# Optimization experiments

Measured on AMD Instinct MI355X. Metric: run time of the kernel, lower is better.

## Reference

```python
import jax, jax.numpy as jnp
import numpy as np


def setup_inputs() -> dict:
    key = jax.random.key(0)
    k1, = jax.random.split(key, 1)
    inputs = jax.random.normal(k1, (16, 64, 64, 512), dtype=jnp.float32)
    gamma = jnp.zeros((1,), dtype=jnp.float32)
    return {"inputs": inputs, "gamma": gamma}


def reference(inputs, gamma):
    # inputs: [B, H, W, C] (NHWC)
    B, H, W, C = inputs.shape
    vec_a = inputs.reshape(B, H * W, C)              # [B, N, C], N = H*W
    # channel Gram matrix: aTa[b, i, j] = sum_n a[b, n, i] * a[b, n, j]
    aTa = jnp.einsum('bni,bnj->bij', vec_a, vec_a)    # [B, C, C]
    attn = jax.nn.softmax(aTa, axis=-1)               # softmax over last axis
    # aaTa = attn @ vec_a^T -> [B, C, N]; transpose -> [B, N, C]
    aaTa = jnp.einsum('bij,bnj->bni', attn, vec_a)    # [B, N, C]
    aaTa = aaTa.reshape(B, H, W, C)
    return gamma * aaTa + inputs
```

## Files before the change

kernel.cpp:

```cpp
#include <hip/hip_runtime.h>

#define BATCH 16
#define NPIX  4096
#define CCH   512
#define NSPLIT 4
#define KSPL  (NPIX / NSPLIT)

using bf16x8   = __attribute__((ext_vector_type(8))) __bf16;
using floatx4  = __attribute__((ext_vector_type(4))) float;
using ushort8v = __attribute__((ext_vector_type(8))) unsigned short;

static __device__ __forceinline__ unsigned short f2bf(float f) {
    unsigned u = __builtin_bit_cast(unsigned, f);
    unsigned r = 0x7fffu + ((u >> 16) & 1u);
    return (unsigned short)((u + r) >> 16);
}

static __device__ __forceinline__ bf16x8 ld_frag(const unsigned short* p) {
    return __builtin_bit_cast(bf16x8, *(const ushort8v*)p);
}

static __device__ __forceinline__ void gld16(const unsigned short* g, unsigned short* l) {
    __builtin_amdgcn_global_load_lds(
        (const __attribute__((address_space(1))) void*)g,
        (__attribute__((address_space(3))) void*)l,
        16, 0, 0);
}

__global__ __launch_bounds__(256) void k_cvt(const float* __restrict__ inp,
                                             unsigned short* __restrict__ Abf,
                                             unsigned short* __restrict__ AT) {
    __shared__ unsigned short sN[64 * 68];
    const int bn = blockIdx.x;
    const int bc = blockIdx.y;
    const int b  = blockIdx.z;
    const int t  = threadIdx.x;
    const int n0 = bn * 64, c0 = bc * 64;
    const float* ip = inp + ((size_t)b * NPIX + n0) * CCH + c0;
    unsigned short* op = Abf + ((size_t)b * NPIX + n0) * CCH + c0;

#pragma unroll
    for (int r = 0; r < 4; ++r) {
        int n  = r * 16 + (t >> 4);
        int c4 = (t & 15) * 4;
        float4 v = *(const float4*)(ip + (size_t)n * CCH + c4);
        uint2 w;
        w.x = (unsigned)f2bf(v.x) | ((unsigned)f2bf(v.y) << 16);
        w.y = (unsigned)f2bf(v.z) | ((unsigned)f2bf(v.w) << 16);
        *(uint2*)(op + (size_t)n * CCH + c4) = w;
        *(uint2*)&sN[n * 68 + c4] = w;
    }
    __syncthreads();

    const int cp = t >> 3;
    const int ng = (t & 7) * 8;
    ushort8v o0, o1;
#pragma unroll
    for (int k = 0; k < 8; ++k) {
        unsigned d = *(const unsigned*)&sN[(ng + k) * 68 + cp * 2];
        o0[k] = (unsigned short)(d & 0xffffu);
        o1[k] = (unsigned short)(d >> 16);
    }
    unsigned short* tp = AT + ((size_t)b * CCH + c0) * NPIX + n0;
    *(ushort8v*)(tp + (size_t)(cp * 2)     * NPIX + ng) = o0;
    *(ushort8v*)(tp + (size_t)(cp * 2 + 1) * NPIX + ng) = o1;
}

__global__ __launch_bounds__(256) void k_ata(const unsigned short* __restrict__ AT,
                                             float* __restrict__ Sp) {
    __shared__ unsigned short sA[128 * 32];
    __shared__ unsigned short sB[128 * 32];
    const int bi = blockIdx.x, bj = blockIdx.y;
    const int b = blockIdx.z & (BATCH - 1), s = blockIdx.z >> 4;
    const unsigned short* pa = AT + ((size_t)b * CCH + bi * 128) * NPIX + s * KSPL;
    const unsigned short* pb = AT + ((size_t)b * CCH + bj * 128) * NPIX + s * KSPL;
    const int tid = threadIdx.x, lane = tid & 63, wave = tid >> 6;
    const int lrow = lane >> 2;
    const int lk   = (lane & 3) * 8;

    floatx4 acc[2][8];
#pragma unroll
    for (int tm = 0; tm < 2; ++tm)
#pragma unroll
        for (int tn = 0; tn < 8; ++tn)
            acc[tm][tn] = floatx4{0.f, 0.f, 0.f, 0.f};

    for (int k0 = 0; k0 < KSPL; k0 += 32) {
#pragma unroll
        for (int i = 0; i < 2; ++i) {
            const int r = wave * 32 + i * 16;
            gld16(pa + (size_t)(r + lrow) * NPIX + k0 + lk, &sA[r * 32]);
            gld16(pb + (size_t)(r + lrow) * NPIX + k0 + lk, &sB[r * 32]);
        }
        __syncthreads();

        const int kq = (lane >> 4) * 8;
        bf16x8 af[2], bv[8];
#pragma unroll
        for (int tm = 0; tm < 2; ++tm)
            af[tm] = ld_frag(&sA[(wave * 32 + tm * 16 + (lane & 15)) * 32 + kq]);
#pragma unroll
        for (int tn = 0; tn < 8; ++tn)
            bv[tn] = ld_frag(&sB[(tn * 16 + (lane & 15)) * 32 + kq]);
#pragma unroll
        for (int tm = 0; tm < 2; ++tm)
#pragma unroll
            for (int tn = 0; tn < 8; ++tn)
                acc[tm][tn] = __builtin_amdgcn_mfma_f32_16x16x32_bf16(
                    af[tm], bv[tn], acc[tm][tn], 0, 0, 0);
        __syncthreads();
    }

    float* Sb = Sp + (((size_t)s * BATCH + b) * CCH + bi * 128) * CCH + bj * 128;
#pragma unroll
    for (int tm = 0; tm < 2; ++tm)
#pragma unroll
        for (int tn = 0; tn < 8; ++tn)
#pragma unroll
            for (int r = 0; r < 4; ++r) {
                int irow = wave * 32 + tm * 16 + (lane >> 4) * 4 + r;
                int jcol = tn * 16 + (lane & 15);
                Sb[(size_t)irow * CCH + jcol] = acc[tm][tn][r];
            }
}

__global__ __launch_bounds__(256) void k_softmax(const float* __restrict__ Sp,
                                                 unsigned short* __restrict__ P) {
    __shared__ float red[6];
    const size_t row = blockIdx.x;
    const size_t str = (size_t)BATCH * CCH * CCH;
    const float* p = Sp + row * CCH;
    const int tid = threadIdx.x, lane = tid & 63, wave = tid >> 6;

    float x0 = p[tid] + p[str + tid] + p[2 * str + tid] + p[3 * str + tid];
    float x1 = p[tid + 256] + p[str + tid + 256] + p[2 * str + tid + 256] + p[3 * str + tid + 256];
    float m = fmaxf(x0, x1);
#pragma unroll
    for (int o = 32; o; o >>= 1) m = fmaxf(m, __shfl_xor(m, o, 64));
    if (lane == 0) red[wave] = m;
    __syncthreads();
    if (tid == 0) red[4] = fmaxf(fmaxf(red[0], red[1]), fmaxf(red[2], red[3]));
    __syncthreads();
    m = red[4];

    float e0 = __expf(x0 - m), e1 = __expf(x1 - m);
    float sum = e0 + e1;
#pragma unroll
    for (int o = 32; o; o >>= 1) sum += __shfl_xor(sum, o, 64);
    if (lane == 0) red[wave] = sum;
    __syncthreads();
    if (tid == 0) red[5] = red[0] + red[1] + red[2] + red[3];
    __syncthreads();
    float inv = 1.0f / red[5];

    P[row * CCH + tid]       = f2bf(e0 * inv);
    P[row * CCH + tid + 256] = f2bf(e1 * inv);
}

__global__ __launch_bounds__(256) void k_av(const unsigned short* __restrict__ Abf,
                                            const unsigned short* __restrict__ P,
                                            const float* __restrict__ inp,
                                            const float* __restrict__ gamma,
                                            float* __restrict__ out) {
    __shared__ unsigned short sA[128 * 32];
    __shared__ unsigned short sB[128 * 32];
    const int bn = blockIdx.x, bi = blockIdx.y, b = blockIdx.z;
    const unsigned short* pa = Abf + ((size_t)b * NPIX + bn * 128) * CCH;
    const unsigned short* pb = P + ((size_t)b * CCH + bi * 128) * CCH;
    const int tid = threadIdx.x, lane = tid & 63, wave = tid >> 6;
    const int lrow = lane >> 2;
    const int lk   = (lane & 3) * 8;
    const float g = gamma[0];

    floatx4 acc[2][8];
#pragma unroll
    for (int tm = 0; tm < 2; ++tm)
#pragma unroll
        for (int tn = 0; tn < 8; ++tn)
            acc[tm][tn] = floatx4{0.f, 0.f, 0.f, 0.f};

    for (int k0 = 0; k0 < CCH; k0 += 32) {
#pragma unroll
        for (int i = 0; i < 2; ++i) {
            const int r = wave * 32 + i * 16;
            gld16(pa + (size_t)(r + lrow) * CCH + k0 + lk, &sA[r * 32]);
            gld16(pb + (size_t)(r + lrow) * CCH + k0 + lk, &sB[r * 32]);
        }
        __syncthreads();

        const int kq = (lane >> 4) * 8;
        bf16x8 af[2], bv[8];
#pragma unroll
        for (int tm = 0; tm < 2; ++tm)
            af[tm] = ld_frag(&sA[(wave * 32 + tm * 16 + (lane & 15)) * 32 + kq]);
#pragma unroll
        for (int tn = 0; tn < 8; ++tn)
            bv[tn] = ld_frag(&sB[(tn * 16 + (lane & 15)) * 32 + kq]);
#pragma unroll
        for (int tm = 0; tm < 2; ++tm)
#pragma unroll
            for (int tn = 0; tn < 8; ++tn)
                acc[tm][tn] = __builtin_amdgcn_mfma_f32_16x16x32_bf16(
                    af[tm], bv[tn], acc[tm][tn], 0, 0, 0);
        __syncthreads();
    }

    float* Ob = out + ((size_t)b * NPIX + bn * 128) * CCH + bi * 128;
    const float* Ib = inp + ((size_t)b * NPIX + bn * 128) * CCH + bi * 128;
#pragma unroll
    for (int tm = 0; tm < 2; ++tm)
#pragma unroll
        for (int tn = 0; tn < 8; ++tn)
#pragma unroll
            for (int r = 0; r < 4; ++r) {
                int nrow = wave * 32 + tm * 16 + (lane >> 4) * 4 + r;
                int icol = tn * 16 + (lane & 15);
                size_t o = (size_t)nrow * CCH + icol;
                Ob[o] = g * acc[tm][tn][r] + Ib[o];
            }
}

extern "C" void kernel_launch(void* const* d_in, const int* in_sizes, int n_in,
                              void* d_out, int out_size, void* d_ws, size_t ws_size,
                              hipStream_t stream) {
    const float* inp   = (const float*)d_in[0];
    const float* gamma = (const float*)d_in[1];
    float* out = (float*)d_out;

    char* ws = (char*)d_ws;
    unsigned short* Abf = (unsigned short*)ws;
    unsigned short* AT  = (unsigned short*)(ws + (size_t)67108864);
    float*          Sp  = (float*)(ws + (size_t)134217728);
    unsigned short* P   = (unsigned short*)(ws + (size_t)201326592);

    k_cvt<<<dim3(NPIX / 64, CCH / 64, BATCH), 256, 0, stream>>>(inp, Abf, AT);
    k_ata<<<dim3(4, 4, BATCH * NSPLIT), 256, 0, stream>>>(AT, Sp);
    k_softmax<<<BATCH * CCH, 256, 0, stream>>>(Sp, P);
    k_av<<<dim3(NPIX / 128, CCH / 128, BATCH), 256, 0, stream>>>(Abf, P, inp, gamma, out);
}
```

Baseline: 459.0 us.

## Exploit Gram symmetry, store bf16 partials in fragment layout, widen split-K

```diff
diff --git a/kernel.cpp b/kernel.cpp
--- a/kernel.cpp
+++ b/kernel.cpp
@@ -3,23 +3,27 @@
 #define BATCH 16
 #define NPIX  4096
 #define CCH   512
-#define NSPLIT 4
+#define NSPLIT 8
 #define KSPL  (NPIX / NSPLIT)
+#define NUT   10
 
 using bf16x8   = __attribute__((ext_vector_type(8))) __bf16;
 using floatx4  = __attribute__((ext_vector_type(4))) float;
 using ushort8v = __attribute__((ext_vector_type(8))) unsigned short;
+using ushort4v = __attribute__((ext_vector_type(4))) unsigned short;
 
 static __device__ __forceinline__ unsigned short f2bf(float f) {
     unsigned u = __builtin_bit_cast(unsigned, f);
     unsigned r = 0x7fffu + ((u >> 16) & 1u);
     return (unsigned short)((u + r) >> 16);
 }
-
+static __device__ __forceinline__ float bf2f(unsigned short v) {
+    unsigned u = ((unsigned)v) << 16;
+    return __builtin_bit_cast(float, u);
+}
 static __device__ __forceinline__ bf16x8 ld_frag(const unsigned short* p) {
     return __builtin_bit_cast(bf16x8, *(const ushort8v*)p);
 }
-
 static __device__ __forceinline__ void gld16(const unsigned short* g, unsigned short* l) {
     __builtin_amdgcn_global_load_lds(
         (const __attribute__((address_space(1))) void*)g,
@@ -30,25 +34,24 @@
 __global__ __launch_bounds__(256) void k_cvt(const float* __restrict__ inp,
                                              unsigned short* __restrict__ Abf,
                                              unsigned short* __restrict__ AT) {
-    __shared__ unsigned short sN[64 * 68];
-    const int bn = blockIdx.x;
-    const int bc = blockIdx.y;
-    const int b  = blockIdx.z;
+    __shared__ unsigned short sN[64 * 66];
+    const int bn = blockIdx.x, bc = blockIdx.y, b = blockIdx.z;
     const int t  = threadIdx.x;
     const int n0 = bn * 64, c0 = bc * 64;
     const float* ip = inp + ((size_t)b * NPIX + n0) * CCH + c0;
     unsigned short* op = Abf + ((size_t)b * NPIX + n0) * CCH + c0;
 
 #pragma unroll
-    for (int r = 0; r < 4; ++r) {
-        int n  = r * 16 + (t >> 4);
-        int c4 = (t & 15) * 4;
-        float4 v = *(const float4*)(ip + (size_t)n * CCH + c4);
-        uint2 w;
-        w.x = (unsigned)f2bf(v.x) | ((unsigned)f2bf(v.y) << 16);
-        w.y = (unsigned)f2bf(v.z) | ((unsigned)f2bf(v.w) << 16);
-        *(uint2*)(op + (size_t)n * CCH + c4) = w;
-        *(uint2*)&sN[n * 68 + c4] = w;
+    for (int r = 0; r < 2; ++r) {
+        int n  = r * 32 + (t >> 3);
+        int c8 = (t & 7) * 8;
+        float4 v0 = *(const float4*)(ip + (size_t)n * CCH + c8);
+        float4 v1 = *(const float4*)(ip + (size_t)n * CCH + c8 + 4);
+        ushort8v w;
+        w[0] = f2bf(v0.x); w[1] = f2bf(v0.y); w[2] = f2bf(v0.z); w[3] = f2bf(v0.w);
+        w[4] = f2bf(v1.x); w[5] = f2bf(v1.y); w[6] = f2bf(v1.z); w[7] = f2bf(v1.w);
+        *(ushort8v*)(op + (size_t)n * CCH + c8) = w;
+        *(ushort8v*)&sN[n * 66 + c8] = w;
     }
     __syncthreads();
 
@@ -57,7 +60,7 @@
     ushort8v o0, o1;
 #pragma unroll
     for (int k = 0; k < 8; ++k) {
-        unsigned d = *(const unsigned*)&sN[(ng + k) * 68 + cp * 2];
+        unsigned d = *(const unsigned*)&sN[(ng + k) * 66 + cp * 2];
         o0[k] = (unsigned short)(d & 0xffffu);
         o1[k] = (unsigned short)(d >> 16);
     }
@@ -67,13 +70,15 @@
 }
 
 __global__ __launch_bounds__(256) void k_ata(const unsigned short* __restrict__ AT,
-                                             float* __restrict__ Sp) {
+                                             unsigned short* __restrict__ Sp) {
     __shared__ unsigned short sA[128 * 32];
     __shared__ unsigned short sB[128 * 32];
-    const int bi = blockIdx.x, bj = blockIdx.y;
-    const int b = blockIdx.z & (BATCH - 1), s = blockIdx.z >> 4;
-    const unsigned short* pa = AT + ((size_t)b * CCH + bi * 128) * NPIX + s * KSPL;
-    const unsigned short* pb = AT + ((size_t)b * CCH + bj * 128) * NPIX + s * KSPL;
+    const int u = blockIdx.x, s = blockIdx.y, b = blockIdx.z;
+    const int ti = (u < 4) ? 0 : (u < 7) ? 1 : (u < 9) ? 2 : 3;
+    const int u0 = ti * 5 - (ti * (ti + 1)) / 2;
+    const int tj = ti + (u - u0);
+    const unsigned short* pa = AT + ((size_t)b * CCH + ti * 128) * NPIX + s * KSPL;
+    const unsigned short* pb = AT + ((size_t)b * CCH + tj * 128) * NPIX + s * KSPL;
     const int tid = threadIdx.x, lane = tid & 63, wave = tid >> 6;
     const int lrow = lane >> 2;
     const int lk   = (lane & 3) * 8;
@@ -111,30 +116,48 @@
         __syncthreads();
     }
 
-    float* Sb = Sp + (((size_t)s * BATCH + b) * CCH + bi * 128) * CCH + bj * 128;
-#pragma unroll
-    for (int tm = 0; tm < 2; ++tm)
-#pragma unroll
-        for (int tn = 0; tn < 8; ++tn)
-#pragma unroll
-            for (int r = 0; r < 4; ++r) {
-                int irow = wave * 32 + tm * 16 + (lane >> 4) * 4 + r;
-                int jcol = tn * 16 + (lane & 15);
-                Sb[(size_t)irow * CCH + jcol] = acc[tm][tn][r];
-            }
-}
-
-__global__ __launch_bounds__(256) void k_softmax(const float* __restrict__ Sp,
+    unsigned short* Tb = Sp + ((((size_t)s * BATCH + b) * NUT + u) << 14);
+#pragma unroll
+    for (int tm = 0; tm < 2; ++tm)
+#pragma unroll
+        for (int tn = 0; tn < 8; ++tn) {
+            ushort4v w;
+#pragma unroll
+            for (int r = 0; r < 4; ++r) w[r] = f2bf(acc[tm][tn][r]);
+            *(ushort4v*)&Tb[((((wave * 2 + tm) * 8 + tn) * 64) + lane) * 4] = w;
+        }
+}
+
+__global__ __launch_bounds__(256) void k_softmax(const unsigned short* __restrict__ Sp,
                                                  unsigned short* __restrict__ P) {
     __shared__ float red[6];
-    const size_t row = blockIdx.x;
-    const size_t str = (size_t)BATCH * CCH * CCH;
-    const float* p = Sp + row * CCH;
+    const int row = blockIdx.x;
+    const int b = row >> 9, i = row & 511;
     const int tid = threadIdx.x, lane = tid & 63, wave = tid >> 6;
-
-    float x0 = p[tid] + p[str + tid] + p[2 * str + tid] + p[3 * str + tid];
-    float x1 = p[tid + 256] + p[str + tid + 256] + p[2 * str + tid + 256] + p[3 * str + tid + 256];
-    float m = fmaxf(x0, x1);
+    const size_t sstr = (size_t)BATCH * NUT * 16384;
+
+    float x[2];
+#pragma unroll
+    for (int e = 0; e < 2; ++e) {
+        const int j  = tid + e * 256;
+        const int ti = i >> 7, tj = j >> 7;
+        const int il = i & 127, jl = j & 127;
+        const bool sw = ti > tj;
+        const int a  = sw ? tj : ti;
+        const int cm = sw ? ti : tj;
+        const int u  = a * 4 + cm - ((a * (a + 1)) >> 1);
+        const int rr = sw ? jl : il;
+        const int cc = sw ? il : jl;
+        const int off = ((((rr >> 4) * 8 + (cc >> 4)) * 64) +
+                         ((rr >> 2) & 3) * 16 + (cc & 15)) * 4 + (rr & 3);
+        const size_t base = (((size_t)b * NUT + u) << 14) + off;
+        float v = 0.f;
+#pragma unroll
+        for (int s = 0; s < NSPLIT; ++s) v += bf2f(Sp[base + s * sstr]);
+        x[e] = v;
+    }
+
+    float m = fmaxf(x[0], x[1]);
 #pragma unroll
     for (int o = 32; o; o >>= 1) m = fmaxf(m, __shfl_xor(m, o, 64));
     if (lane == 0) red[wave] = m;
@@ -143,7 +166,7 @@
     __syncthreads();
     m = red[4];
 
-    float e0 = __expf(x0 - m), e1 = __expf(x1 - m);
+    float e0 = __expf(x[0] - m), e1 = __expf(x[1] - m);
     float sum = e0 + e1;
 #pragma unroll
     for (int o = 32; o; o >>= 1) sum += __shfl_xor(sum, o, 64);
@@ -153,8 +176,8 @@
     __syncthreads();
     float inv = 1.0f / red[5];
 
-    P[row * CCH + tid]       = f2bf(e0 * inv);
-    P[row * CCH + tid + 256] = f2bf(e1 * inv);
+    P[(size_t)row * CCH + tid]       = f2bf(e0 * inv);
+    P[(size_t)row * CCH + tid + 256] = f2bf(e1 * inv);
 }
 
 __global__ __launch_bounds__(256) void k_av(const unsigned short* __restrict__ Abf,
@@ -230,11 +253,11 @@
     char* ws = (char*)d_ws;
     unsigned short* Abf = (unsigned short*)ws;
     unsigned short* AT  = (unsigned short*)(ws + (size_t)67108864);
-    float*          Sp  = (float*)(ws + (size_t)134217728);
-    unsigned short* P   = (unsigned short*)(ws + (size_t)201326592);
+    unsigned short* Sp  = (unsigned short*)(ws + (size_t)134217728);
+    unsigned short* P   = (unsigned short*)(ws + (size_t)134217728 + 41943040);
 
     k_cvt<<<dim3(NPIX / 64, CCH / 64, BATCH), 256, 0, stream>>>(inp, Abf, AT);
-    k_ata<<<dim3(4, 4, BATCH * NSPLIT), 256, 0, stream>>>(AT, Sp);
+    k_ata<<<dim3(NUT, NSPLIT, BATCH), 256, 0, stream>>>(AT, Sp);
     k_softmax<<<BATCH * CCH, 256, 0, stream>>>(Sp, P);
     k_av<<<dim3(NPIX / 128, CCH / 128, BATCH), 256, 0, stream>>>(Abf, P, inp, gamma, out);
 }
```

After: 414.3 us. -9.7%, faster.
